# Kernel optimization log

Measured on AMD Instinct MI355X. Metric: run time of the kernel, lower is better.

## Reference

```python
import jax, jax.numpy as jnp
import numpy as np

EPSILON = 1.5  # quality-tolerance threshold from init_kwargs
NEG_INF = -1000000000.0


def setup_inputs() -> dict:
    key = jax.random.key(0)
    k1, k2, k3 = jax.random.split(key, 3)
    B, S, D, E = 4, 4096, 2048, 64
    return {
        "hidden_states": jax.random.normal(k1, (B, S, D), dtype=jnp.float32),
        "gate_W": jax.random.normal(k2, (E, D), dtype=jnp.float32),  # nn.Linear weight [out,in]
        "secret_projection": jax.random.normal(k3, (D, E), dtype=jnp.float32),
        "top_k": 2,
    }


def reference(hidden_states, gate_W, secret_projection, top_k):
    # raw gate logits: Linear without bias -> x @ W^T
    raw_logits = jnp.einsum("bsd,ed->bse", hidden_states, gate_W)
    # watermark bias via secret LSH projection
    watermark_bias = jnp.einsum("bsd,de->bse", hidden_states, secret_projection)
    # indifference zone: experts whose logit is within epsilon of the max
    max_logits = jnp.max(raw_logits, axis=-1, keepdims=True)
    safe_mask = raw_logits >= max_logits - EPSILON
    modified_scores = jnp.where(safe_mask, watermark_bias, jnp.asarray(NEG_INF, raw_logits.dtype))
    # top-k over watermark-preferred safe experts
    _, selected_experts = jax.lax.top_k(modified_scores, top_k)
    # gather original logits at selected experts, softmax over the k slots
    router_logits = jnp.take_along_axis(raw_logits, selected_experts, axis=-1)
    routing_weights = jax.nn.softmax(router_logits, axis=-1)
    return routing_weights, selected_experts
```

## Files before the change

kernel.cpp:

```cpp
#include <hip/hip_runtime.h>
#include <stdint.h>


#define DDIM 2048
#define NEXP 64
#define NCOL 128
#define BM   128
#define NEG_INF   -1000000000.0f
#define MARGIN_RAW 0.01f
#define MARGIN_WM  0.05f

typedef __attribute__((ext_vector_type(8))) short bf16x8;
typedef __attribute__((ext_vector_type(4))) float f32x4;

union BFrag { bf16x8 v; uint32_t w[4]; uint4 q; };

__device__ inline void split8(const float* a, bf16x8* hi, bf16x8* lo) {
    BFrag h, l;
    #pragma unroll
    for (int p = 0; p < 4; ++p) {
        const uint32_t u0 = __float_as_uint(a[2*p]);
        const uint32_t u1 = __float_as_uint(a[2*p+1]);
        const uint32_t h0 = (u0 + 0x7FFFu + ((u0 >> 16) & 1u)) >> 16;
        const uint32_t h1 = (u1 + 0x7FFFu + ((u1 >> 16) & 1u)) >> 16;
        const float r0 = a[2*p]   - __uint_as_float(h0 << 16);
        const float r1 = a[2*p+1] - __uint_as_float(h1 << 16);
        const uint32_t v0 = __float_as_uint(r0);
        const uint32_t v1 = __float_as_uint(r1);
        const uint32_t l0 = (v0 + 0x7FFFu + ((v0 >> 16) & 1u)) >> 16;
        const uint32_t l1 = (v1 + 0x7FFFu + ((v1 >> 16) & 1u)) >> 16;
        h.w[p] = h0 | (h1 << 16);
        l.w[p] = l0 | (l1 << 16);
    }
    *hi = h.v; *lo = l.v;
}

__global__ void prep_b(const float* __restrict__ gateW, const float* __restrict__ secret,
                       uint4* __restrict__ wsB) {
    const int kstep = blockIdx.x;
    const int s = threadIdx.x >> 6;
    const int l = threadIdx.x & 63;
    const int col = s * 16 + (l & 15);
    const int kb  = kstep * 32 + (l >> 4) * 8;
    float v[8];
    if (col < NEXP) {
        #pragma unroll
        for (int j = 0; j < 8; ++j) v[j] = gateW[(size_t)col * DDIM + kb + j];
    } else {
        #pragma unroll
        for (int j = 0; j < 8; ++j) v[j] = secret[(size_t)(kb + j) * NEXP + (col - NEXP)];
    }
    bf16x8 hi, lo; split8(v, &hi, &lo);
    const size_t base = (size_t)(kstep * 8 + s) * 128 + l;
    BFrag t;
    t.v = hi; wsB[base]      = t.q;
    t.v = lo; wsB[base + 64] = t.q;
}

template <int KSPLIT>
__global__ __launch_bounds__(256, 2)
void gemm_split(const float* __restrict__ x, const uint4* __restrict__ wsB,
                float* __restrict__ wsP, int ntok) {
    const int KQ  = DDIM / KSPLIT;
    const int NKS = KQ / 32;
    const int bx = blockIdx.x;
    const int q  = bx & (KSPLIT - 1);
    const int mb = bx / KSPLIT;
    const int w  = threadIdx.x >> 6;
    const int l  = threadIdx.x & 63;
    const int rl = l & 15;
    const int kg = l >> 4;
    const int rowb = mb * BM + w * 32;

    f32x4 acc[2][8];
    #pragma unroll
    for (int i = 0; i < 2; ++i)
        #pragma unroll
        for (int j = 0; j < 8; ++j) acc[i][j] = (f32x4){0.f, 0.f, 0.f, 0.f};

    const float* xr0 = x + (size_t)(rowb + rl) * DDIM + q * KQ + kg * 8;
    const float* xr1 = xr0 + (size_t)16 * DDIM;
    const uint4* bp  = wsB + (size_t)(q * NKS * 8) * 128 + l;

    for (int ts = 0; ts < NKS; ++ts) {
        bf16x8 bh[8], bl[8];
        #pragma unroll
        for (int s = 0; s < 8; ++s) {
            BFrag t;
            t.q = bp[(size_t)(ts * 8 + s) * 128];      bh[s] = t.v;
            t.q = bp[(size_t)(ts * 8 + s) * 128 + 64]; bl[s] = t.v;
        }
        const float4 a0 = *reinterpret_cast<const float4*>(xr0 + ts * 32);
        const float4 a1 = *reinterpret_cast<const float4*>(xr0 + ts * 32 + 4);
        const float4 a2 = *reinterpret_cast<const float4*>(xr1 + ts * 32);
        const float4 a3 = *reinterpret_cast<const float4*>(xr1 + ts * 32 + 4);
        const float v0[8] = {a0.x, a0.y, a0.z, a0.w, a1.x, a1.y, a1.z, a1.w};
        const float v1[8] = {a2.x, a2.y, a2.z, a2.w, a3.x, a3.y, a3.z, a3.w};
        bf16x8 ah0, al0, ah1, al1;
        split8(v0, &ah0, &al0);
        split8(v1, &ah1, &al1);

        #pragma unroll
        for (int s = 0; s < 8; ++s) {
            acc[0][s] = __builtin_amdgcn_mfma_f32_16x16x32_bf16(ah0, bh[s], acc[0][s], 0, 0, 0);
            acc[0][s] = __builtin_amdgcn_mfma_f32_16x16x32_bf16(ah0, bl[s], acc[0][s], 0, 0, 0);
            acc[0][s] = __builtin_amdgcn_mfma_f32_16x16x32_bf16(al0, bh[s], acc[0][s], 0, 0, 0);
            acc[1][s] = __builtin_amdgcn_mfma_f32_16x16x32_bf16(ah1, bh[s], acc[1][s], 0, 0, 0);
            acc[1][s] = __builtin_amdgcn_mfma_f32_16x16x32_bf16(ah1, bl[s], acc[1][s], 0, 0, 0);
            acc[1][s] = __builtin_amdgcn_mfma_f32_16x16x32_bf16(al1, bh[s], acc[1][s], 0, 0, 0);
        }
    }

    const size_t MN = (size_t)ntok * NCOL;
    #pragma unroll
    for (int m = 0; m < 2; ++m) {
        const int tokb = rowb + m * 16 + kg * 4;
        #pragma unroll
        for (int s = 0; s < 8; ++s)
            #pragma unroll
            for (int r = 0; r < 4; ++r)
                wsP[(size_t)q * MN + (size_t)(tokb + r) * NCOL + s * 16 + rl] = acc[m][s][r];
    }
}

__device__ inline void wave_argmax(float& bv, int& bi) {
    #pragma unroll
    for (int off = 32; off; off >>= 1) {
        const float ov = __shfl_xor(bv, off);
        const int   oi = __shfl_xor(bi, off);
        if (ov > bv || (ov == bv && oi < bi)) { bv = ov; bi = oi; }
    }
}

template <int KSPLIT>
__global__ void router_k(const float* __restrict__ wsP,
                         const float* __restrict__ x,
                         const float* __restrict__ gateW,
                         const float* __restrict__ secret,
                         float* __restrict__ out, int ntok) {
    const int t = blockIdx.x * 4 + (threadIdx.x >> 6);
    const int e = threadIdx.x & 63;
    const size_t MN = (size_t)ntok * NCOL;

    float raw = 0.f, wm = 0.f;
    #pragma unroll
    for (int q = 0; q < KSPLIT; ++q) {
        raw += wsP[(size_t)q * MN + (size_t)t * NCOL + e];
        wm  += wsP[(size_t)q * MN + (size_t)t * NCOL + NEXP + e];
    }

    float rmax = raw;
    #pragma unroll
    for (int off = 32; off; off >>= 1) rmax = fmaxf(rmax, __shfl_xor(rmax, off));

    if (__any(fabsf(raw - (rmax - 1.5f)) < MARGIN_RAW)) {
        float s = 0.f;
        const float4* xr = reinterpret_cast<const float4*>(x + (size_t)t * DDIM);
        const float4* wr = reinterpret_cast<const float4*>(gateW + (size_t)e * DDIM);
        for (int k = 0; k < DDIM / 4; ++k) {
            const float4 a = xr[k], b = wr[k];
            s = fmaf(a.x, b.x, s); s = fmaf(a.y, b.y, s);
            s = fmaf(a.z, b.z, s); s = fmaf(a.w, b.w, s);
        }
        raw = s;
        rmax = raw;
        #pragma unroll
        for (int off = 32; off; off >>= 1) rmax = fmaxf(rmax, __shfl_xor(rmax, off));
    }

    const bool safe = (raw >= rmax - 1.5f);
    float m = safe ? wm : NEG_INF;

    float v1 = m; int e1 = e;
    wave_argmax(v1, e1);
    float v2 = (e == e1) ? -3.0e38f : m; int e2 = e;
    wave_argmax(v2, e2);
    float v3 = (e == e1 || e == e2) ? -3.0e38f : m; int e3 = e;
    wave_argmax(v3, e3);

    const bool wmRisk = (v2 > NEG_INF + 1.0f && v1 - v2 < MARGIN_WM) ||
                        (v3 > NEG_INF + 1.0f && v2 - v3 < MARGIN_WM);
    if (__any(wmRisk)) {
        float s = 0.f;
        const float* xr = x + (size_t)t * DDIM;
        for (int k = 0; k < DDIM; k += 4) {
            s = fmaf(xr[k],     secret[(size_t)(k)     * NEXP + e], s);
            s = fmaf(xr[k + 1], secret[(size_t)(k + 1) * NEXP + e], s);
            s = fmaf(xr[k + 2], secret[(size_t)(k + 2) * NEXP + e], s);
            s = fmaf(xr[k + 3], secret[(size_t)(k + 3) * NEXP + e], s);
        }
        m = safe ? s : NEG_INF;
        v1 = m; e1 = e;  wave_argmax(v1, e1);
        v2 = (e == e1) ? -3.0e38f : m; e2 = e;  wave_argmax(v2, e2);
    }

    const float l1 = __shfl(raw, e1);
    const float l2 = __shfl(raw, e2);

    if (e == 0) {
        const float mm = fmaxf(l1, l2);
        const float x1 = expf(l1 - mm), x2 = expf(l2 - mm);
        const float inv = 1.0f / (x1 + x2);
        out[(size_t)t * 2 + 0] = x1 * inv;
        out[(size_t)t * 2 + 1] = x2 * inv;
        out[(size_t)2 * ntok + t * 2 + 0] = (float)e1;
        out[(size_t)2 * ntok + t * 2 + 1] = (float)e2;
    }
}

extern "C" void kernel_launch(void* const* d_in, const int* in_sizes, int n_in,
                              void* d_out, int out_size, void* d_ws, size_t ws_size,
                              hipStream_t stream) {
    const float* x      = (const float*)d_in[0];
    const float* gateW  = (const float*)d_in[1];
    const float* secret = (const float*)d_in[2];
    float* out = (float*)d_out;

    const int ntok = in_sizes[0] / DDIM;
    uint4* wsB = (uint4*)d_ws;
    float* wsP = (float*)((char*)d_ws + (2u << 20));
    const size_t MN4 = (size_t)ntok * NCOL * 4;

    prep_b<<<64, 512, 0, stream>>>(gateW, secret, wsB);

    if (ws_size >= (2u << 20) + 4 * MN4) {
        gemm_split<4><<<(ntok / BM) * 4, 256, 0, stream>>>(x, wsB, wsP, ntok);
        router_k<4><<<ntok / 4, 256, 0, stream>>>(wsP, x, gateW, secret, out, ntok);
    } else if (ws_size >= (2u << 20) + 2 * MN4) {
        gemm_split<2><<<(ntok / BM) * 2, 256, 0, stream>>>(x, wsB, wsP, ntok);
        router_k<2><<<ntok / 4, 256, 0, stream>>>(wsP, x, gateW, secret, out, ntok);
    } else {
        gemm_split<1><<<(ntok / BM), 256, 0, stream>>>(x, wsB, wsP, ntok);
        router_k<1><<<ntok / 4, 256, 0, stream>>>(wsP, x, gateW, secret, out, ntok);
    }
}
```

Measured before the change: 98.88 us.

## Replace global split-K partials with in-block split-K LDS reduction and truncation split

The GEMM now gives each block 32 tokens. Waves pair up over two K halves and reduce their partials through shared memory, so the old multi-way partial buffer in global memory is gone and the router reads a single logit row. The activation hi/lo split now truncates instead of rounding to nearest, which cuts ALU work per element. To cover the larger error from truncation, the fallback margins are widened, which may send more tokens down the exact fp32 recompute paths. Those fallback dot products now use four independent accumulators.

```diff
diff --git a/kernel.cpp b/kernel.cpp
--- a/kernel.cpp
+++ b/kernel.cpp
@@ -4,18 +4,17 @@
 
 #define DDIM 2048
 #define NEXP 64
-#define NCOL 128
-#define BM   128
-#define NEG_INF   -1000000000.0f
-#define MARGIN_RAW 0.01f
-#define MARGIN_WM  0.05f
+#define NEG_INF  -1000000000.0f
+#define MRG_RAW  0.04f
+#define MRG_WM   0.15f
+#define RST      130
 
 typedef __attribute__((ext_vector_type(8))) short bf16x8;
 typedef __attribute__((ext_vector_type(4))) float f32x4;
 
 union BFrag { bf16x8 v; uint32_t w[4]; uint4 q; };
 
-__device__ inline void split8(const float* a, bf16x8* hi, bf16x8* lo) {
+__device__ inline void split8_rne(const float* a, bf16x8* hi, bf16x8* lo) {
     BFrag h, l;
     #pragma unroll
     for (int p = 0; p < 4; ++p) {
@@ -35,6 +34,20 @@
     *hi = h.v; *lo = l.v;
 }
 
+__device__ inline void split8t(const float* a, bf16x8* hi, bf16x8* lo) {
+    BFrag h, l;
+    #pragma unroll
+    for (int p = 0; p < 4; ++p) {
+        const uint32_t u0 = __float_as_uint(a[2*p]);
+        const uint32_t u1 = __float_as_uint(a[2*p+1]);
+        h.w[p] = (u0 >> 16) | (u1 & 0xFFFF0000u);
+        const float r0 = a[2*p]   - __uint_as_float(u0 & 0xFFFF0000u);
+        const float r1 = a[2*p+1] - __uint_as_float(u1 & 0xFFFF0000u);
+        l.w[p] = (__float_as_uint(r0) >> 16) | (__float_as_uint(r1) & 0xFFFF0000u);
+    }
+    *hi = h.v; *lo = l.v;
+}
+
 __global__ void prep_b(const float* __restrict__ gateW, const float* __restrict__ secret,
                        uint4* __restrict__ wsB) {
     const int kstep = blockIdx.x;
@@ -50,119 +63,104 @@
         #pragma unroll
         for (int j = 0; j < 8; ++j) v[j] = secret[(size_t)(kb + j) * NEXP + (col - NEXP)];
     }
-    bf16x8 hi, lo; split8(v, &hi, &lo);
+    bf16x8 hi, lo; split8_rne(v, &hi, &lo);
     const size_t base = (size_t)(kstep * 8 + s) * 128 + l;
     BFrag t;
     t.v = hi; wsB[base]      = t.q;
     t.v = lo; wsB[base + 64] = t.q;
 }
 
-template <int KSPLIT>
-__global__ __launch_bounds__(256, 2)
-void gemm_split(const float* __restrict__ x, const uint4* __restrict__ wsB,
-                float* __restrict__ wsP, int ntok) {
-    const int KQ  = DDIM / KSPLIT;
-    const int NKS = KQ / 32;
-    const int bx = blockIdx.x;
-    const int q  = bx & (KSPLIT - 1);
-    const int mb = bx / KSPLIT;
-    const int w  = threadIdx.x >> 6;
-    const int l  = threadIdx.x & 63;
-    const int rl = l & 15;
-    const int kg = l >> 4;
-    const int rowb = mb * BM + w * 32;
-
-    f32x4 acc[2][8];
-    #pragma unroll
-    for (int i = 0; i < 2; ++i)
-        #pragma unroll
-        for (int j = 0; j < 8; ++j) acc[i][j] = (f32x4){0.f, 0.f, 0.f, 0.f};
-
-    const float* xr0 = x + (size_t)(rowb + rl) * DDIM + q * KQ + kg * 8;
-    const float* xr1 = xr0 + (size_t)16 * DDIM;
-    const uint4* bp  = wsB + (size_t)(q * NKS * 8) * 128 + l;
-
-    for (int ts = 0; ts < NKS; ++ts) {
-        bf16x8 bh[8], bl[8];
+__global__ __launch_bounds__(256, 3)
+void gemm32(const float* __restrict__ x, const bf16x8* __restrict__ wsB,
+            float* __restrict__ wsL, int ntok)
+{
+    __shared__ float red[2][16 * RST];
+
+    const int tid = threadIdx.x;
+    const int w = tid >> 6;
+    const int p = w & 1;
+    const int h = w >> 1;
+    const int l = tid & 63;
+    const int c = l & 15;
+    const int g = l >> 4;
+    const int rowbase = blockIdx.x * 32 + p * 16;
+
+    f32x4 acc[8];
+    #pragma unroll
+    for (int s = 0; s < 8; ++s) acc[s] = (f32x4){0.f, 0.f, 0.f, 0.f};
+
+    const float* xr = x + (size_t)(rowbase + c) * DDIM + h * 1024 + g * 8;
+    const bf16x8* bp = wsB + ((size_t)h * 32 * 8) * 128 + l;
+
+    for (int ts = 0; ts < 32; ++ts) {
+        bf16x8 bq[16];
         #pragma unroll
         for (int s = 0; s < 8; ++s) {
-            BFrag t;
-            t.q = bp[(size_t)(ts * 8 + s) * 128];      bh[s] = t.v;
-            t.q = bp[(size_t)(ts * 8 + s) * 128 + 64]; bl[s] = t.v;
-        }
-        const float4 a0 = *reinterpret_cast<const float4*>(xr0 + ts * 32);
-        const float4 a1 = *reinterpret_cast<const float4*>(xr0 + ts * 32 + 4);
-        const float4 a2 = *reinterpret_cast<const float4*>(xr1 + ts * 32);
-        const float4 a3 = *reinterpret_cast<const float4*>(xr1 + ts * 32 + 4);
-        const float v0[8] = {a0.x, a0.y, a0.z, a0.w, a1.x, a1.y, a1.z, a1.w};
-        const float v1[8] = {a2.x, a2.y, a2.z, a2.w, a3.x, a3.y, a3.z, a3.w};
-        bf16x8 ah0, al0, ah1, al1;
-        split8(v0, &ah0, &al0);
-        split8(v1, &ah1, &al1);
+            bq[2*s]     = bp[(size_t)(ts * 8 + s) * 128];
+            bq[2*s + 1] = bp[(size_t)(ts * 8 + s) * 128 + 64];
+        }
+        const float4 a0 = *reinterpret_cast<const float4*>(xr + ts * 32);
+        const float4 a1 = *reinterpret_cast<const float4*>(xr + ts * 32 + 4);
+        const float va[8] = {a0.x, a0.y, a0.z, a0.w, a1.x, a1.y, a1.z, a1.w};
+        bf16x8 ah, al;
+        split8t(va, &ah, &al);
 
         #pragma unroll
         for (int s = 0; s < 8; ++s) {
-            acc[0][s] = __builtin_amdgcn_mfma_f32_16x16x32_bf16(ah0, bh[s], acc[0][s], 0, 0, 0);
-            acc[0][s] = __builtin_amdgcn_mfma_f32_16x16x32_bf16(ah0, bl[s], acc[0][s], 0, 0, 0);
-            acc[0][s] = __builtin_amdgcn_mfma_f32_16x16x32_bf16(al0, bh[s], acc[0][s], 0, 0, 0);
-            acc[1][s] = __builtin_amdgcn_mfma_f32_16x16x32_bf16(ah1, bh[s], acc[1][s], 0, 0, 0);
-            acc[1][s] = __builtin_amdgcn_mfma_f32_16x16x32_bf16(ah1, bl[s], acc[1][s], 0, 0, 0);
-            acc[1][s] = __builtin_amdgcn_mfma_f32_16x16x32_bf16(al1, bh[s], acc[1][s], 0, 0, 0);
-        }
-    }
-
-    const size_t MN = (size_t)ntok * NCOL;
-    #pragma unroll
-    for (int m = 0; m < 2; ++m) {
-        const int tokb = rowb + m * 16 + kg * 4;
+            acc[s] = __builtin_amdgcn_mfma_f32_16x16x32_bf16(ah, bq[2*s],     acc[s], 0, 0, 0);
+            acc[s] = __builtin_amdgcn_mfma_f32_16x16x32_bf16(ah, bq[2*s + 1], acc[s], 0, 0, 0);
+            acc[s] = __builtin_amdgcn_mfma_f32_16x16x32_bf16(al, bq[2*s],     acc[s], 0, 0, 0);
+        }
+    }
+
+    if (h == 1) {
+        float* L = red[p];
         #pragma unroll
         for (int s = 0; s < 8; ++s)
             #pragma unroll
             for (int r = 0; r < 4; ++r)
-                wsP[(size_t)q * MN + (size_t)(tokb + r) * NCOL + s * 16 + rl] = acc[m][s][r];
-    }
-}
-
-__device__ inline void wave_argmax(float& bv, int& bi) {
-    #pragma unroll
-    for (int off = 32; off; off >>= 1) {
-        const float ov = __shfl_xor(bv, off);
-        const int   oi = __shfl_xor(bi, off);
-        if (ov > bv || (ov == bv && oi < bi)) { bv = ov; bi = oi; }
-    }
-}
-
-template <int KSPLIT>
-__global__ void router_k(const float* __restrict__ wsP,
-                         const float* __restrict__ x,
-                         const float* __restrict__ gateW,
-                         const float* __restrict__ secret,
-                         float* __restrict__ out, int ntok) {
+                L[(g * 4 + r) * RST + s * 16 + c] = acc[s][r];
+    }
+    __syncthreads();
+    if (h == 0) {
+        const float* L = red[p];
+        #pragma unroll
+        for (int s = 0; s < 8; ++s)
+            #pragma unroll
+            for (int r = 0; r < 4; ++r) {
+                const float v = acc[s][r] + L[(g * 4 + r) * RST + s * 16 + c];
+                wsL[(size_t)(rowbase + g * 4 + r) * 128 + s * 16 + c] = v;
+            }
+    }
+}
+
+__global__ __launch_bounds__(256, 4)
+void router_k(const float* __restrict__ wsL,
+              const float* __restrict__ x,
+              const float* __restrict__ gateW,
+              const float* __restrict__ secret,
+              float* __restrict__ out, int ntok)
+{
     const int t = blockIdx.x * 4 + (threadIdx.x >> 6);
     const int e = threadIdx.x & 63;
-    const size_t MN = (size_t)ntok * NCOL;
-
-    float raw = 0.f, wm = 0.f;
-    #pragma unroll
-    for (int q = 0; q < KSPLIT; ++q) {
-        raw += wsP[(size_t)q * MN + (size_t)t * NCOL + e];
-        wm  += wsP[(size_t)q * MN + (size_t)t * NCOL + NEXP + e];
-    }
+
+    float raw = wsL[(size_t)t * 128 + e];
+    float wm  = wsL[(size_t)t * 128 + NEXP + e];
 
     float rmax = raw;
     #pragma unroll
     for (int off = 32; off; off >>= 1) rmax = fmaxf(rmax, __shfl_xor(rmax, off));
 
-    if (__any(fabsf(raw - (rmax - 1.5f)) < MARGIN_RAW)) {
-        float s = 0.f;
+    if (__any(fabsf(raw - (rmax - 1.5f)) < MRG_RAW)) {
+        float s0 = 0.f, s1 = 0.f, s2 = 0.f, s3 = 0.f;
         const float4* xr = reinterpret_cast<const float4*>(x + (size_t)t * DDIM);
         const float4* wr = reinterpret_cast<const float4*>(gateW + (size_t)e * DDIM);
         for (int k = 0; k < DDIM / 4; ++k) {
             const float4 a = xr[k], b = wr[k];
-            s = fmaf(a.x, b.x, s); s = fmaf(a.y, b.y, s);
-            s = fmaf(a.z, b.z, s); s = fmaf(a.w, b.w, s);
-        }
-        raw = s;
+            s0 = fmaf(a.x, b.x, s0); s1 = fmaf(a.y, b.y, s1);
+            s2 = fmaf(a.z, b.z, s2); s3 = fmaf(a.w, b.w, s3);
+        }
+        raw = (s0 + s1) + (s2 + s3);
         rmax = raw;
         #pragma unroll
         for (int off = 32; off; off >>= 1) rmax = fmaxf(rmax, __shfl_xor(rmax, off));
@@ -172,26 +170,48 @@
     float m = safe ? wm : NEG_INF;
 
     float v1 = m; int e1 = e;
-    wave_argmax(v1, e1);
+    #pragma unroll
+    for (int off = 32; off; off >>= 1) {
+        const float ov = __shfl_xor(v1, off); const int oi = __shfl_xor(e1, off);
+        if (ov > v1 || (ov == v1 && oi < e1)) { v1 = ov; e1 = oi; }
+    }
     float v2 = (e == e1) ? -3.0e38f : m; int e2 = e;
-    wave_argmax(v2, e2);
+    #pragma unroll
+    for (int off = 32; off; off >>= 1) {
+        const float ov = __shfl_xor(v2, off); const int oi = __shfl_xor(e2, off);
+        if (ov > v2 || (ov == v2 && oi < e2)) { v2 = ov; e2 = oi; }
+    }
     float v3 = (e == e1 || e == e2) ? -3.0e38f : m; int e3 = e;
-    wave_argmax(v3, e3);
-
-    const bool wmRisk = (v2 > NEG_INF + 1.0f && v1 - v2 < MARGIN_WM) ||
-                        (v3 > NEG_INF + 1.0f && v2 - v3 < MARGIN_WM);
+    #pragma unroll
+    for (int off = 32; off; off >>= 1) {
+        const float ov = __shfl_xor(v3, off); const int oi = __shfl_xor(e3, off);
+        if (ov > v3 || (ov == v3 && oi < e3)) { v3 = ov; e3 = oi; }
+    }
+
+    const bool wmRisk = (v2 > NEG_INF + 1.0f && v1 - v2 < MRG_WM) ||
+                        (v3 > NEG_INF + 1.0f && v2 - v3 < MRG_WM);
     if (__any(wmRisk)) {
-        float s = 0.f;
+        float s0 = 0.f, s1 = 0.f, s2 = 0.f, s3 = 0.f;
         const float* xr = x + (size_t)t * DDIM;
         for (int k = 0; k < DDIM; k += 4) {
-            s = fmaf(xr[k],     secret[(size_t)(k)     * NEXP + e], s);
-            s = fmaf(xr[k + 1], secret[(size_t)(k + 1) * NEXP + e], s);
-            s = fmaf(xr[k + 2], secret[(size_t)(k + 2) * NEXP + e], s);
-            s = fmaf(xr[k + 3], secret[(size_t)(k + 3) * NEXP + e], s);
-        }
-        m = safe ? s : NEG_INF;
-        v1 = m; e1 = e;  wave_argmax(v1, e1);
-        v2 = (e == e1) ? -3.0e38f : m; e2 = e;  wave_argmax(v2, e2);
+            s0 = fmaf(xr[k + 0], secret[(size_t)(k + 0) * NEXP + e], s0);
+            s1 = fmaf(xr[k + 1], secret[(size_t)(k + 1) * NEXP + e], s1);
+            s2 = fmaf(xr[k + 2], secret[(size_t)(k + 2) * NEXP + e], s2);
+            s3 = fmaf(xr[k + 3], secret[(size_t)(k + 3) * NEXP + e], s3);
+        }
+        m = safe ? ((s0 + s1) + (s2 + s3)) : NEG_INF;
+        v1 = m; e1 = e;
+        #pragma unroll
+        for (int off = 32; off; off >>= 1) {
+            const float ov = __shfl_xor(v1, off); const int oi = __shfl_xor(e1, off);
+            if (ov > v1 || (ov == v1 && oi < e1)) { v1 = ov; e1 = oi; }
+        }
+        v2 = (e == e1) ? -3.0e38f : m; e2 = e;
+        #pragma unroll
+        for (int off = 32; off; off >>= 1) {
+            const float ov = __shfl_xor(v2, off); const int oi = __shfl_xor(e2, off);
+            if (ov > v2 || (ov == v2 && oi < e2)) { v2 = ov; e2 = oi; }
+        }
     }
 
     const float l1 = __shfl(raw, e1);
@@ -218,19 +238,9 @@
 
     const int ntok = in_sizes[0] / DDIM;
     uint4* wsB = (uint4*)d_ws;
-    float* wsP = (float*)((char*)d_ws + (2u << 20));
-    const size_t MN4 = (size_t)ntok * NCOL * 4;
+    float* wsL = (float*)((char*)d_ws + (2u << 20));
 
     prep_b<<<64, 512, 0, stream>>>(gateW, secret, wsB);
-
-    if (ws_size >= (2u << 20) + 4 * MN4) {
-        gemm_split<4><<<(ntok / BM) * 4, 256, 0, stream>>>(x, wsB, wsP, ntok);
-        router_k<4><<<ntok / 4, 256, 0, stream>>>(wsP, x, gateW, secret, out, ntok);
-    } else if (ws_size >= (2u << 20) + 2 * MN4) {
-        gemm_split<2><<<(ntok / BM) * 2, 256, 0, stream>>>(x, wsB, wsP, ntok);
-        router_k<2><<<ntok / 4, 256, 0, stream>>>(wsP, x, gateW, secret, out, ntok);
-    } else {
-        gemm_split<1><<<(ntok / BM), 256, 0, stream>>>(x, wsB, wsP, ntok);
-        router_k<1><<<ntok / 4, 256, 0, stream>>>(wsP, x, gateW, secret, out, ntok);
-    }
-}
+    gemm32<<<ntok / 32, 256, 0, stream>>>(x, (const bf16x8*)wsB, wsL, ntok);
+    router_k<<<ntok / 4, 256, 0, stream>>>(wsL, x, gateW, secret, out, ntok);
+}
```

New measurement: 117.2 us. 18.6% more time.
